# Kernel tuning notes

Hardware: AMD Instinct MI355X
Metric: run time of the kernel (lower is better)

Reference implementation:

```python
import jax, jax.numpy as jnp
import numpy as np

B, N, M, D = 32, 1024, 256, 512
NEG_INF = -1e9  # keras Softmax mask additive constant


def _length_mask(key, batch, length):
    # realistic padding masks: first L positions valid, L >= length//4
    lens = jax.random.randint(key, (batch,), length // 4, length + 1)
    return jnp.arange(length)[None, :] < lens[:, None]


def setup_inputs() -> dict:
    key = jax.random.key(0)
    k1, k2, k3, k4, k5 = jax.random.split(key, 5)
    context = jax.random.normal(k1, (B, N, D), dtype=jnp.float32)
    query = jax.random.normal(k2, (B, M, D), dtype=jnp.float32)
    c_mask = _length_mask(k3, B, N)
    q_mask = _length_mask(k4, B, M)
    # Dense(units=1, use_bias=False) kernel over concat([q, c, q*c]) -> (3D, 1)
    w = jax.random.normal(k5, (3 * D, 1), dtype=jnp.float32) * (1.0 / np.sqrt(3 * D))
    return {"context": context, "query": query, "c_mask": c_mask, "q_mask": q_mask, "w": w}


def reference(context, query, c_mask, q_mask, w):
    d = context.shape[-1]
    # stack order in original: [q_matrix, c_matrix, q*c]
    w_q = w[:d, 0]
    w_c = w[d:2 * d, 0]
    w_m = w[2 * d:, 0]
    # trilinear similarity S[b,n,m] = q_j.w_q + c_i.w_c + (c_i*q_j).w_m, decomposed
    S = (context @ w_c)[:, :, None] \
        + (query @ w_q)[:, None, :] \
        + jnp.einsum('bnd,bmd->bnm', context * w_m, query)
    # context-direction softmax over query axis (axis=2), masked by q_mask
    A = jax.nn.softmax(jnp.where(q_mask[:, None, :], S, NEG_INF), axis=2)
    # query-direction softmax over context axis (axis=1), masked by c_mask
    Bm = jax.nn.softmax(jnp.where(c_mask[:, :, None], S, NEG_INF), axis=1)
    # context-to-query attention: A @ query -> (b, n, d)
    c2q = jnp.einsum('bnm,bmd->bnd', A, query)
    # query-to-context: (A @ B^T) @ context -> (b, n, d)
    q2c = jnp.einsum('bnk,bjk,bjd->bnd', A, Bm, context)
    out = jnp.concatenate([context, c2q, context * c2q, context * q2c], axis=-1)
    return out
```

## Files before the change

kernel.cpp:

```cpp
#include <hip/hip_runtime.h>
#include <hip/hip_bf16.h>

#define B_ 32
#define N_ 1024
#define M_ 256
#define D_ 512

typedef __attribute__((ext_vector_type(8))) short short8;
typedef __attribute__((ext_vector_type(4))) float f32x4;

#define OFF_S     ((size_t)0)
#define OFF_CTXW  ((size_t)8388608)
#define OFF_ANM   ((size_t)8388608)
#define OFF_BMT   ((size_t)12582912)
#define OFF_QB    ((size_t)16777216)
#define OFF_QT    ((size_t)18874368)
#define OFF_CT    ((size_t)20971520)
#define OFF_CDOT  ((size_t)29360128)
#define OFF_QDOT  ((size_t)29392896)
#define OFF_PMAX  ((size_t)29483008)
#define OFF_PSUM  ((size_t)29614080)
#define OFF_RPMAX ((size_t)29745152)
#define OFF_RPSUM ((size_t)29876224)

__global__ __launch_bounds__(256) void prep_all(
    const float* __restrict__ ctx, const float* __restrict__ qry,
    const float* __restrict__ w,
    __hip_bfloat16* __restrict__ ctxw, __hip_bfloat16* __restrict__ cT,
    float* __restrict__ cdot,
    __hip_bfloat16* __restrict__ qb, __hip_bfloat16* __restrict__ qT,
    float* __restrict__ qdot)
{
    __shared__ float t[64][65];
    const int b = blockIdx.z, d0 = blockIdx.x * 64;
    const int tid = threadIdx.x;
    const float* src;
    __hip_bfloat16* rowdst;
    __hip_bfloat16* trdst;
    float* dotdst;
    int ldt;
    float4 wmv, wdv;
    const int lr16 = tid & 15, rband = tid >> 4;
    const int c = lr16 * 4;
    if (blockIdx.y < N_ / 64) {
        int r0 = blockIdx.y * 64;
        src    = ctx + ((size_t)b * N_ + r0) * D_ + d0;
        rowdst = ctxw + ((size_t)b * N_ + r0) * D_ + d0;
        trdst  = cT + ((size_t)b * D_ + d0) * N_ + r0;
        dotdst = cdot + b * N_ + r0;
        wmv = *(const float4*)(w + 2 * D_ + d0 + c);
        wdv = *(const float4*)(w + D_ + d0 + c);
        ldt = N_;
    } else {
        int r0 = (blockIdx.y - N_ / 64) * 64;
        src    = qry + ((size_t)b * M_ + r0) * D_ + d0;
        rowdst = qb + ((size_t)b * M_ + r0) * D_ + d0;
        trdst  = qT + ((size_t)b * D_ + d0) * M_ + r0;
        dotdst = qdot + b * M_ + r0;
        wmv = (float4){1.f, 1.f, 1.f, 1.f};
        wdv = *(const float4*)(w + d0 + c);
        ldt = M_;
    }
#pragma unroll
    for (int i = 0; i < 4; ++i) {
        int r = i * 16 + rband;
        float4 x = *(const float4*)(src + (size_t)r * D_ + c);
        t[r][c] = x.x; t[r][c + 1] = x.y; t[r][c + 2] = x.z; t[r][c + 3] = x.w;
        __hip_bfloat16 o[4] __attribute__((aligned(8)));
        o[0] = __float2bfloat16(x.x * wmv.x);
        o[1] = __float2bfloat16(x.y * wmv.y);
        o[2] = __float2bfloat16(x.z * wmv.z);
        o[3] = __float2bfloat16(x.w * wmv.w);
        *(ushort4*)(rowdst + (size_t)r * D_ + c) = *(ushort4*)o;
        float p = x.x * wdv.x + x.y * wdv.y + x.z * wdv.z + x.w * wdv.w;
#pragma unroll
        for (int off = 1; off < 16; off <<= 1) p += __shfl_xor(p, off, 64);
        if (lr16 == 0) atomicAdd(dotdst + r, p);
    }
    __syncthreads();
    const int dr = tid >> 2, sseg = tid & 3;
    __hip_bfloat16 o[16] __attribute__((aligned(16)));
#pragma unroll
    for (int j = 0; j < 16; ++j)
        o[j] = __float2bfloat16(t[sseg * 16 + j][dr]);
    __hip_bfloat16* dp = trdst + (size_t)dr * ldt + sseg * 16;
    ((short8*)dp)[0] = ((short8*)o)[0];
    ((short8*)dp)[1] = ((short8*)o)[1];
}


__device__ __forceinline__ void gl2lds16(const __hip_bfloat16* g, __hip_bfloat16* l) {
    __builtin_amdgcn_global_load_lds(
        (const __attribute__((address_space(1))) unsigned int*)g,
        (__attribute__((address_space(3))) unsigned int*)l, 16, 0, 0);
}

template<int KTOT>
__device__ __forceinline__ void mfma128(
    const __hip_bfloat16* __restrict__ Abase, int lda,
    const __hip_bfloat16* __restrict__ Bbase, int ldb,
    __hip_bfloat16* As, __hip_bfloat16* Bs, f32x4 acc[4][4])
{
    const int tid = threadIdx.x;
    const int w = tid >> 6, lane = tid & 63;
    const int quad = lane >> 4, lr = lane & 15;
    const int wr = w >> 1, wc = w & 1;
    const int srow = w * 32 + (lane >> 2);
    const int scol = (lane & 3) * 8;
    const __hip_bfloat16* ga0 = Abase + (size_t)srow * lda + scol;
    const __hip_bfloat16* ga1 = ga0 + (size_t)16 * lda;
    const __hip_bfloat16* gb0 = Bbase + (size_t)srow * ldb + scol;
    const __hip_bfloat16* gb1 = gb0 + (size_t)16 * ldb;
    __hip_bfloat16* la0 = As + w * 1024;
    __hip_bfloat16* la1 = As + w * 1024 + 512;
    __hip_bfloat16* lb0 = Bs + w * 1024;
    __hip_bfloat16* lb1 = Bs + w * 1024 + 512;
    const int aoff = (wr * 64 + lr) * 32 + quad * 8;
    const int boff = (wc * 64 + lr) * 32 + quad * 8;

    for (int k0 = 0; k0 < KTOT; k0 += 32) {
        gl2lds16(ga0, la0); gl2lds16(ga1, la1);
        gl2lds16(gb0, lb0); gl2lds16(gb1, lb1);
        ga0 += 32; ga1 += 32; gb0 += 32; gb1 += 32;
        asm volatile("s_waitcnt vmcnt(0)" ::: "memory");
        __syncthreads();
        short8 a[4], bb[4];
        const short8* ap = (const short8*)(As + aoff);
        const short8* bp = (const short8*)(Bs + boff);
#pragma unroll
        for (int fi = 0; fi < 4; ++fi) a[fi] = ap[fi * 64];
#pragma unroll
        for (int fj = 0; fj < 4; ++fj) bb[fj] = bp[fj * 64];
#pragma unroll
        for (int fi = 0; fi < 4; ++fi)
#pragma unroll
            for (int fj = 0; fj < 4; ++fj)
                acc[fi][fj] = __builtin_amdgcn_mfma_f32_16x16x32_bf16(
                    a[fi], bb[fj], acc[fi][fj], 0, 0, 0);
        __syncthreads();
    }
}

template<int KTOT>
__device__ __forceinline__ void mfma128x2(
    const __hip_bfloat16* __restrict__ Abase, int lda,
    const __hip_bfloat16* __restrict__ B1base,
    const __hip_bfloat16* __restrict__ B2base, int ldb,
    __hip_bfloat16* As, __hip_bfloat16* B1s, __hip_bfloat16* B2s,
    f32x4 acc1[4][4], f32x4 acc2[4][4])
{
    const int tid = threadIdx.x;
    const int w = tid >> 6, lane = tid & 63;
    const int quad = lane >> 4, lr = lane & 15;
    const int wr = w >> 1, wc = w & 1;
    const int srow = w * 32 + (lane >> 2);
    const int scol = (lane & 3) * 8;
    const __hip_bfloat16* ga0 = Abase + (size_t)srow * lda + scol;
    const __hip_bfloat16* ga1 = ga0 + (size_t)16 * lda;
    const __hip_bfloat16* gb10 = B1base + (size_t)srow * ldb + scol;
    const __hip_bfloat16* gb11 = gb10 + (size_t)16 * ldb;
    const __hip_bfloat16* gb20 = B2base + (size_t)srow * ldb + scol;
    const __hip_bfloat16* gb21 = gb20 + (size_t)16 * ldb;
    __hip_bfloat16* la0 = As + w * 1024;
    __hip_bfloat16* la1 = la0 + 512;
    __hip_bfloat16* lb10 = B1s + w * 1024;
    __hip_bfloat16* lb11 = lb10 + 512;
    __hip_bfloat16* lb20 = B2s + w * 1024;
    __hip_bfloat16* lb21 = lb20 + 512;
    const int aoff = (wr * 64 + lr) * 32 + quad * 8;
    const int boff = (wc * 64 + lr) * 32 + quad * 8;

    for (int k0 = 0; k0 < KTOT; k0 += 32) {
        gl2lds16(ga0, la0); gl2lds16(ga1, la1);
        gl2lds16(gb10, lb10); gl2lds16(gb11, lb11);
        gl2lds16(gb20, lb20); gl2lds16(gb21, lb21);
        ga0 += 32; ga1 += 32; gb10 += 32; gb11 += 32; gb20 += 32; gb21 += 32;
        asm volatile("s_waitcnt vmcnt(0)" ::: "memory");
        __syncthreads();
        short8 a[4], b1[4], b2[4];
        const short8* ap = (const short8*)(As + aoff);
        const short8* bp1 = (const short8*)(B1s + boff);
        const short8* bp2 = (const short8*)(B2s + boff);
#pragma unroll
        for (int fi = 0; fi < 4; ++fi) a[fi] = ap[fi * 64];
#pragma unroll
        for (int fj = 0; fj < 4; ++fj) { b1[fj] = bp1[fj * 64]; b2[fj] = bp2[fj * 64]; }
#pragma unroll
        for (int fi = 0; fi < 4; ++fi)
#pragma unroll
            for (int fj = 0; fj < 4; ++fj) {
                acc1[fi][fj] = __builtin_amdgcn_mfma_f32_16x16x32_bf16(
                    a[fi], b1[fj], acc1[fi][fj], 0, 0, 0);
                acc2[fi][fj] = __builtin_amdgcn_mfma_f32_16x16x32_bf16(
                    a[fi], b2[fj], acc2[fi][fj], 0, 0, 0);
            }
        __syncthreads();
    }
}

#define ACC_INIT(acc) \
    _Pragma("unroll") for (int i_ = 0; i_ < 4; ++i_) \
    _Pragma("unroll") for (int j_ = 0; j_ < 4; ++j_) acc[i_][j_] = (f32x4){0.f, 0.f, 0.f, 0.f};

#define EPI_IDX const int tid = threadIdx.x, lane = tid & 63, quad = lane >> 4, lr = lane & 15; \
    const int wr = tid >> 7, wc = (tid >> 6) & 1;

__global__ __launch_bounds__(256) void s_gemm_stats(
    const __hip_bfloat16* __restrict__ ctxw, const __hip_bfloat16* __restrict__ qryb,
    const float* __restrict__ cdot, const float* __restrict__ qdot,
    const int* __restrict__ q_mask, const int* __restrict__ c_mask,
    float* __restrict__ S,
    float* __restrict__ rpmax, float* __restrict__ rpsum,
    float* __restrict__ pmax, float* __restrict__ psum)
{
    __shared__ __align__(16) __hip_bfloat16 As[4096], Bs[4096];
    const int b = blockIdx.z, n0 = blockIdx.y * 128, m0 = blockIdx.x * 128;
    f32x4 acc[4][4];
    ACC_INIT(acc)
    mfma128<512>(ctxw + ((size_t)b * N_ + n0) * D_, D_,
                 qryb + ((size_t)b * M_ + m0) * D_, D_, As, Bs, acc);
    EPI_IDX
    float cd[4][4]; int cmv[4][4];
#pragma unroll
    for (int fi = 0; fi < 4; ++fi)
#pragma unroll
        for (int r = 0; r < 4; ++r) {
            int n = n0 + wr * 64 + fi * 16 + quad * 4 + r;
            cd[fi][r] = cdot[b * N_ + n];
            cmv[fi][r] = c_mask[b * N_ + n];
        }
    float qd[4]; int qmv[4];
#pragma unroll
    for (int fj = 0; fj < 4; ++fj) {
        int m = m0 + wc * 64 + fj * 16 + lr;
        qd[fj] = qdot[b * M_ + m];
        qmv[fj] = q_mask[b * M_ + m];
    }
#pragma unroll
    for (int fi = 0; fi < 4; ++fi)
#pragma unroll
        for (int r = 0; r < 4; ++r) {
            int n = n0 + wr * 64 + fi * 16 + quad * 4 + r;
            size_t rowoff = ((size_t)b * N_ + n) * M_;
#pragma unroll
            for (int fj = 0; fj < 4; ++fj) {
                int m = m0 + wc * 64 + fj * 16 + lr;
                S[rowoff + m] = acc[fi][fj][r] + cd[fi][r] + qd[fj];
            }
        }
    const int part = blockIdx.x * 2 + wc;
#pragma unroll
    for (int fi = 0; fi < 4; ++fi)
#pragma unroll
        for (int r = 0; r < 4; ++r) {
            float xs[4], mx = -1e30f;
#pragma unroll
            for (int fj = 0; fj < 4; ++fj) {
                xs[fj] = qmv[fj] ? (acc[fi][fj][r] + cd[fi][r] + qd[fj]) : -1e9f;
                mx = fmaxf(mx, xs[fj]);
            }
#pragma unroll
            for (int off = 1; off < 16; off <<= 1)
                mx = fmaxf(mx, __shfl_xor(mx, off, 64));
            float se = 0.f;
#pragma unroll
            for (int fj = 0; fj < 4; ++fj) se += __expf(xs[fj] - mx);
#pragma unroll
            for (int off = 1; off < 16; off <<= 1)
                se += __shfl_xor(se, off, 64);
            if (lr == 0) {
                int n = n0 + wr * 64 + fi * 16 + quad * 4 + r;
                rpmax[((size_t)b * N_ + n) * 4 + part] = mx;
                rpsum[((size_t)b * N_ + n) * 4 + part] = se;
            }
        }
    const int ch = blockIdx.y * 2 + wr;
#pragma unroll
    for (int fj = 0; fj < 4; ++fj) {
        float mx = -1e30f;
#pragma unroll
        for (int fi = 0; fi < 4; ++fi)
#pragma unroll
            for (int r = 0; r < 4; ++r) {
                float x = cmv[fi][r] ? (acc[fi][fj][r] + cd[fi][r] + qd[fj]) : -1e9f;
                mx = fmaxf(mx, x);
            }
        mx = fmaxf(mx, __shfl_xor(mx, 16, 64));
        mx = fmaxf(mx, __shfl_xor(mx, 32, 64));
        float se = 0.f;
#pragma unroll
        for (int fi = 0; fi < 4; ++fi)
#pragma unroll
            for (int r = 0; r < 4; ++r) {
                float x = cmv[fi][r] ? (acc[fi][fj][r] + cd[fi][r] + qd[fj]) : -1e9f;
                se += __expf(x - mx);
            }
        se += __shfl_xor(se, 16, 64);
        se += __shfl_xor(se, 32, 64);
        if (lane < 16) {
            int m = m0 + wc * 64 + fj * 16 + lr;
            pmax[((size_t)b * 16 + ch) * M_ + m] = mx;
            psum[((size_t)b * 16 + ch) * M_ + m] = se;
        }
    }
}

__global__ __launch_bounds__(256) void q2cpart_mfma(
    const __hip_bfloat16* __restrict__ ctxT, const __hip_bfloat16* __restrict__ BmT,
    __hip_bfloat16* __restrict__ Q2CT)
{
    __shared__ __align__(16) __hip_bfloat16 As[4096], Bs[4096];
    const int b = blockIdx.z, d0 = blockIdx.y * 128, m0 = blockIdx.x * 128;
    f32x4 acc[4][4];
    ACC_INIT(acc)
    mfma128<1024>(ctxT + ((size_t)b * D_ + d0) * N_, N_,
                  BmT + ((size_t)b * M_ + m0) * N_, N_, As, Bs, acc);
    EPI_IDX
#pragma unroll
    for (int fi = 0; fi < 4; ++fi) {
#pragma unroll
        for (int r = 0; r < 4; ++r) {
            int d = d0 + wr * 64 + fi * 16 + quad * 4 + r;
#pragma unroll
            for (int fj = 0; fj < 4; ++fj) {
                int m = m0 + wc * 64 + fj * 16 + lr;
                Q2CT[((size_t)b * D_ + d) * M_ + m] = __float2bfloat16(acc[fi][fj][r]);
            }
        }
    }
}

__global__ __launch_bounds__(256) void out_fused_mfma(
    const __hip_bfloat16* __restrict__ Anm, const __hip_bfloat16* __restrict__ qryT,
    const __hip_bfloat16* __restrict__ Q2CT, const float* __restrict__ ctx,
    float* __restrict__ out)
{
    __shared__ __align__(16) __hip_bfloat16 As[4096], B1s[4096], B2s[4096];
    const int b = blockIdx.z, n0 = blockIdx.y * 128, d0 = blockIdx.x * 128;
    f32x4 acc1[4][4], acc2[4][4];
    ACC_INIT(acc1)
    ACC_INIT(acc2)
    mfma128x2<256>(Anm + ((size_t)b * N_ + n0) * M_, M_,
                   qryT + ((size_t)b * D_ + d0) * M_,
                   Q2CT + ((size_t)b * D_ + d0) * M_, M_,
                   As, B1s, B2s, acc1, acc2);
    EPI_IDX
#pragma unroll
    for (int fi = 0; fi < 4; ++fi) {
#pragma unroll
        for (int r = 0; r < 4; ++r) {
            int n = n0 + wr * 64 + fi * 16 + quad * 4 + r;
            size_t ibase = ((size_t)b * N_ + n) * D_;
            size_t obase = ((size_t)b * N_ + n) * (4 * D_);
#pragma unroll
            for (int fj = 0; fj < 4; ++fj) {
                int d = d0 + wc * 64 + fj * 16 + lr;
                float c = ctx[ibase + d];
                float v1 = acc1[fi][fj][r];
                float v2 = acc2[fi][fj][r];
                out[obase + d] = c;
                out[obase + D_ + d] = v1;
                out[obase + 2 * D_ + d] = c * v1;
                out[obase + 3 * D_ + d] = c * v2;
            }
        }
    }
}

__global__ __launch_bounds__(256) void normalize_kernel(
    const float* __restrict__ S, __hip_bfloat16* __restrict__ Anm,
    __hip_bfloat16* __restrict__ BmT,
    const int* __restrict__ q_mask, const int* __restrict__ c_mask,
    const float* __restrict__ pmax, const float* __restrict__ psum,
    const float* __restrict__ rpmax, const float* __restrict__ rpsum)
{
    __shared__ float t[64][65];
    __shared__ float cmx_s[64], cinv_s[64], rmx_s[64], rinv_s[64];
    const int b = blockIdx.z, n0 = blockIdx.y * 64, m0 = blockIdx.x * 64;
    const int tid = threadIdx.x;
    if (tid < 64) {
        int m = m0 + tid;
        float mx = -1e30f;
#pragma unroll
        for (int ch = 0; ch < 16; ++ch)
            mx = fmaxf(mx, pmax[((size_t)b * 16 + ch) * M_ + m]);
        float sm = 0.f;
#pragma unroll
        for (int ch = 0; ch < 16; ++ch)
            sm += psum[((size_t)b * 16 + ch) * M_ + m] *
                  __expf(pmax[((size_t)b * 16 + ch) * M_ + m] - mx);
        cmx_s[tid] = mx; cinv_s[tid] = 1.0f / sm;
    } else if (tid < 128) {
        int rl = tid - 64;
        size_t row = (size_t)b * N_ + n0 + rl;
        float mx = -1e30f;
#pragma unroll
        for (int p = 0; p < 4; ++p)
            mx = fmaxf(mx, rpmax[row * 4 + p]);
        float sm = 0.f;
#pragma unroll
        for (int p = 0; p < 4; ++p)
            sm += rpsum[row * 4 + p] * __expf(rpmax[row * 4 + p] - mx);
        rmx_s[rl] = mx; rinv_s[rl] = 1.0f / sm;
    }
    __syncthreads();
    const int lr16 = tid & 15, rband = tid >> 4;
    const int c = lr16 * 4;
    int4 qm4 = *(const int4*)(q_mask + b * M_ + m0 + c);
    float cmx0 = cmx_s[c], cmx1 = cmx_s[c + 1], cmx2 = cmx_s[c + 2], cmx3 = cmx_s[c + 3];
    float ci0 = cinv_s[c], ci1 = cinv_s[c + 1], ci2 = cinv_s[c + 2], ci3 = cinv_s[c + 3];
#pragma unroll
    for (int i = 0; i < 4; ++i) {
        int r = i * 16 + rband;
        int n = n0 + r;
        int cm = c_mask[b * N_ + n];
        float rmx = rmx_s[r], rinv = rinv_s[r];
        size_t idx = ((size_t)b * N_ + n) * M_ + m0 + c;
        float4 s4 = *(const float4*)(S + idx);
        __hip_bfloat16 av[4] __attribute__((aligned(8)));
        av[0] = __float2bfloat16(qm4.x ? __expf(s4.x - rmx) * rinv : 0.f);
        av[1] = __float2bfloat16(qm4.y ? __expf(s4.y - rmx) * rinv : 0.f);
        av[2] = __float2bfloat16(qm4.z ? __expf(s4.z - rmx) * rinv : 0.f);
        av[3] = __float2bfloat16(qm4.w ? __expf(s4.w - rmx) * rinv : 0.f);
        *(ushort4*)(Anm + idx) = *(ushort4*)av;
        t[r][c]     = cm ? __expf(s4.x - cmx0) * ci0 : 0.f;
        t[r][c + 1] = cm ? __expf(s4.y - cmx1) * ci1 : 0.f;
        t[r][c + 2] = cm ? __expf(s4.z - cmx2) * ci2 : 0.f;
        t[r][c + 3] = cm ? __expf(s4.w - cmx3) * ci3 : 0.f;
    }
    __syncthreads();
    const int mr = tid >> 2, sseg = tid & 3;
    __hip_bfloat16 o[16] __attribute__((aligned(16)));
#pragma unroll
    for (int j = 0; j < 16; ++j)
        o[j] = __float2bfloat16(t[sseg * 16 + j][mr]);
    __hip_bfloat16* dp = BmT + ((size_t)b * M_ + m0 + mr) * N_ + n0 + sseg * 16;
    ((short8*)dp)[0] = ((short8*)o)[0];
    ((short8*)dp)[1] = ((short8*)o)[1];
}

extern "C" void kernel_launch(void* const* d_in, const int* in_sizes, int n_in,
                              void* d_out, int out_size, void* d_ws, size_t ws_size,
                              hipStream_t stream) {
    const float* ctx   = (const float*)d_in[0];
    const float* qry   = (const float*)d_in[1];
    const int*   cmask = (const int*)d_in[2];
    const int*   qmask = (const int*)d_in[3];
    const float* w     = (const float*)d_in[4];
    float* out = (float*)d_out;
    float* ws  = (float*)d_ws;

    float* S = ws + OFF_S;
    __hip_bfloat16* ctxw = (__hip_bfloat16*)(ws + OFF_CTXW);
    __hip_bfloat16* Anm  = (__hip_bfloat16*)(ws + OFF_ANM);
    __hip_bfloat16* BmT  = (__hip_bfloat16*)(ws + OFF_BMT);
    __hip_bfloat16* qb   = (__hip_bfloat16*)(ws + OFF_QB);
    __hip_bfloat16* Q2CT = (__hip_bfloat16*)(ws + OFF_QB);
    __hip_bfloat16* qT   = (__hip_bfloat16*)(ws + OFF_QT);
    __hip_bfloat16* cT   = (__hip_bfloat16*)(ws + OFF_CT);
    float* cdot = ws + OFF_CDOT;
    float* qdot = ws + OFF_QDOT;
    float* pmax = ws + OFF_PMAX;
    float* psum = ws + OFF_PSUM;
    float* rpmax = ws + OFF_RPMAX;
    float* rpsum = ws + OFF_RPSUM;

    hipMemsetAsync(cdot, 0, (size_t)(B_ * N_ + B_ * M_) * sizeof(float), stream);

    dim3 gp(D_ / 64, (N_ + M_) / 64, B_);
    prep_all<<<gp, 256, 0, stream>>>(ctx, qry, w, ctxw, cT, cdot, qb, qT, qdot);

    dim3 gS(M_ / 128, N_ / 128, B_);
    s_gemm_stats<<<gS, 256, 0, stream>>>(ctxw, qb, cdot, qdot, qmask, cmask,
                                         S, rpmax, rpsum, pmax, psum);

    dim3 gN(M_ / 64, N_ / 64, B_);
    normalize_kernel<<<gN, 256, 0, stream>>>(S, Anm, BmT, qmask, cmask,
                                             pmax, psum, rpmax, rpsum);

    dim3 gP(M_ / 128, D_ / 128, B_);
    q2cpart_mfma<<<gP, 256, 0, stream>>>(cT, BmT, Q2CT);

    dim3 gO(D_ / 128, N_ / 128, B_);
    out_fused_mfma<<<gO, 256, 0, stream>>>(Anm, qT, Q2CT, ctx, out);
}
```

Baseline: 482.0 us.

## Fuse full-row softmax into S GEMM, store bf16 numerators instead of fp32 S

The score GEMM now gives each block a full 128x256 row tile with 512 threads, so it can finish the row-softmax max and sum in-block and write unnormalized exp numerators as bf16 rather than an fp32 S matrix. Row normalization (1/sum) is deferred to the output kernel's epilogue, and the column softmax is rebuilt from the stored numerators by rescaling with exp(rowmax - colmax). This removes the fp32 S round trip and halves the intermediate traffic. The costs are a larger block with fewer blocks in the grid, and some precision loss, because the column softmax is now derived from bf16 numerators that can underflow where the row max dominates.

After: 473.0 us. Within noise of the previous version (-1.9%).

```diff
diff --git a/kernel.cpp b/kernel.cpp
--- a/kernel.cpp
+++ b/kernel.cpp
@@ -9,9 +9,8 @@
 typedef __attribute__((ext_vector_type(8))) short short8;
 typedef __attribute__((ext_vector_type(4))) float f32x4;
 
-#define OFF_S     ((size_t)0)
+#define OFF_ANUM  ((size_t)0)
 #define OFF_CTXW  ((size_t)8388608)
-#define OFF_ANM   ((size_t)8388608)
 #define OFF_BMT   ((size_t)12582912)
 #define OFF_QB    ((size_t)16777216)
 #define OFF_QT    ((size_t)18874368)
@@ -20,8 +19,8 @@
 #define OFF_QDOT  ((size_t)29392896)
 #define OFF_PMAX  ((size_t)29483008)
 #define OFF_PSUM  ((size_t)29614080)
-#define OFF_RPMAX ((size_t)29745152)
-#define OFF_RPSUM ((size_t)29876224)
+#define OFF_RMAX  ((size_t)29745152)
+#define OFF_RINV  ((size_t)29876224)
 
 __global__ __launch_bounds__(256) void prep_all(
     const float* __restrict__ ctx, const float* __restrict__ qry,
@@ -202,24 +201,56 @@
     _Pragma("unroll") for (int i_ = 0; i_ < 4; ++i_) \
     _Pragma("unroll") for (int j_ = 0; j_ < 4; ++j_) acc[i_][j_] = (f32x4){0.f, 0.f, 0.f, 0.f};
 
-#define EPI_IDX const int tid = threadIdx.x, lane = tid & 63, quad = lane >> 4, lr = lane & 15; \
-    const int wr = tid >> 7, wc = (tid >> 6) & 1;
-
-__global__ __launch_bounds__(256) void s_gemm_stats(
+__global__ __launch_bounds__(512) void s_gemm_full(
     const __hip_bfloat16* __restrict__ ctxw, const __hip_bfloat16* __restrict__ qryb,
     const float* __restrict__ cdot, const float* __restrict__ qdot,
     const int* __restrict__ q_mask, const int* __restrict__ c_mask,
-    float* __restrict__ S,
-    float* __restrict__ rpmax, float* __restrict__ rpsum,
+    __hip_bfloat16* __restrict__ Anum,
+    float* __restrict__ rmax_g, float* __restrict__ rinv_g,
     float* __restrict__ pmax, float* __restrict__ psum)
 {
-    __shared__ __align__(16) __hip_bfloat16 As[4096], Bs[4096];
-    const int b = blockIdx.z, n0 = blockIdx.y * 128, m0 = blockIdx.x * 128;
+    __shared__ __align__(16) __hip_bfloat16 As[4096];
+    __shared__ __align__(16) __hip_bfloat16 Bs[8192];
+    __shared__ float rpm[128][4], rps[128][4];
+    __shared__ float rmx_s[128];
+    const int b = blockIdx.y, n0 = blockIdx.x * 128;
+    const int tid = threadIdx.x;
+    const int w = tid >> 6, lane = tid & 63;
+    const int quad = lane >> 4, lr = lane & 15;
+    const int wr = w >> 2, wc = w & 3;
+    const int srow = tid >> 2, scol = (tid & 3) * 8;
+    const __hip_bfloat16* gA  = ctxw + ((size_t)b * N_ + n0 + srow) * D_ + scol;
+    const __hip_bfloat16* gB0 = qryb + ((size_t)b * M_ + srow) * D_ + scol;
+    const __hip_bfloat16* gB1 = qryb + ((size_t)b * M_ + 128 + srow) * D_ + scol;
+    __hip_bfloat16* la  = As + w * 512;
+    __hip_bfloat16* lb0 = Bs + w * 512;
+    __hip_bfloat16* lb1 = Bs + 4096 + w * 512;
+    const int aoff = (wr * 64 + lr) * 32 + quad * 8;
+    const int boff = (wc * 64 + lr) * 32 + quad * 8;
+
     f32x4 acc[4][4];
     ACC_INIT(acc)
-    mfma128<512>(ctxw + ((size_t)b * N_ + n0) * D_, D_,
-                 qryb + ((size_t)b * M_ + m0) * D_, D_, As, Bs, acc);
-    EPI_IDX
+    for (int k0 = 0; k0 < D_; k0 += 32) {
+        gl2lds16(gA, la); gl2lds16(gB0, lb0); gl2lds16(gB1, lb1);
+        gA += 32; gB0 += 32; gB1 += 32;
+        asm volatile("s_waitcnt vmcnt(0)" ::: "memory");
+        __syncthreads();
+        short8 a[4], bb[4];
+        const short8* ap = (const short8*)(As + aoff);
+        const short8* bp = (const short8*)(Bs + boff);
+#pragma unroll
+        for (int fi = 0; fi < 4; ++fi) a[fi] = ap[fi * 64];
+#pragma unroll
+        for (int fj = 0; fj < 4; ++fj) bb[fj] = bp[fj * 64];
+#pragma unroll
+        for (int fi = 0; fi < 4; ++fi)
+#pragma unroll
+            for (int fj = 0; fj < 4; ++fj)
+                acc[fi][fj] = __builtin_amdgcn_mfma_f32_16x16x32_bf16(
+                    a[fi], bb[fj], acc[fi][fj], 0, 0, 0);
+        __syncthreads();
+    }
+
     float cd[4][4]; int cmv[4][4];
 #pragma unroll
     for (int fi = 0; fi < 4; ++fi)
@@ -232,23 +263,10 @@
     float qd[4]; int qmv[4];
 #pragma unroll
     for (int fj = 0; fj < 4; ++fj) {
-        int m = m0 + wc * 64 + fj * 16 + lr;
+        int m = wc * 64 + fj * 16 + lr;
         qd[fj] = qdot[b * M_ + m];
         qmv[fj] = q_mask[b * M_ + m];
     }
-#pragma unroll
-    for (int fi = 0; fi < 4; ++fi)
-#pragma unroll
-        for (int r = 0; r < 4; ++r) {
-            int n = n0 + wr * 64 + fi * 16 + quad * 4 + r;
-            size_t rowoff = ((size_t)b * N_ + n) * M_;
-#pragma unroll
-            for (int fj = 0; fj < 4; ++fj) {
-                int m = m0 + wc * 64 + fj * 16 + lr;
-                S[rowoff + m] = acc[fi][fj][r] + cd[fi][r] + qd[fj];
-            }
-        }
-    const int part = blockIdx.x * 2 + wc;
 #pragma unroll
     for (int fi = 0; fi < 4; ++fi)
 #pragma unroll
@@ -269,12 +287,38 @@
             for (int off = 1; off < 16; off <<= 1)
                 se += __shfl_xor(se, off, 64);
             if (lr == 0) {
-                int n = n0 + wr * 64 + fi * 16 + quad * 4 + r;
-                rpmax[((size_t)b * N_ + n) * 4 + part] = mx;
-                rpsum[((size_t)b * N_ + n) * 4 + part] = se;
-            }
-        }
-    const int ch = blockIdx.y * 2 + wr;
+                int nl = wr * 64 + fi * 16 + quad * 4 + r;
+                rpm[nl][wc] = mx; rps[nl][wc] = se;
+            }
+        }
+    __syncthreads();
+    if (tid < 128) {
+        float m0v = rpm[tid][0], m1 = rpm[tid][1], m2 = rpm[tid][2], m3 = rpm[tid][3];
+        float mx = fmaxf(fmaxf(m0v, m1), fmaxf(m2, m3));
+        float sm = rps[tid][0] * __expf(m0v - mx) + rps[tid][1] * __expf(m1 - mx)
+                 + rps[tid][2] * __expf(m2 - mx) + rps[tid][3] * __expf(m3 - mx);
+        float inv = 1.0f / sm;
+        rmx_s[tid] = mx;
+        rmax_g[b * N_ + n0 + tid] = mx;
+        rinv_g[b * N_ + n0 + tid] = inv;
+    }
+    __syncthreads();
+#pragma unroll
+    for (int fi = 0; fi < 4; ++fi)
+#pragma unroll
+        for (int r = 0; r < 4; ++r) {
+            int nl = wr * 64 + fi * 16 + quad * 4 + r;
+            float rmx = rmx_s[nl];
+            size_t rowoff = ((size_t)b * N_ + n0 + nl) * M_;
+#pragma unroll
+            for (int fj = 0; fj < 4; ++fj) {
+                int m = wc * 64 + fj * 16 + lr;
+                float sv = acc[fi][fj][r] + cd[fi][r] + qd[fj];
+                float a = qmv[fj] ? __expf(sv - rmx) : 0.f;
+                Anum[rowoff + m] = __float2bfloat16(a);
+            }
+        }
+    const int ch = blockIdx.x * 2 + wr;
 #pragma unroll
     for (int fj = 0; fj < 4; ++fj) {
         float mx = -1e30f;
@@ -298,12 +342,69 @@
         se += __shfl_xor(se, 16, 64);
         se += __shfl_xor(se, 32, 64);
         if (lane < 16) {
-            int m = m0 + wc * 64 + fj * 16 + lr;
+            int m = wc * 64 + fj * 16 + lr;
             pmax[((size_t)b * 16 + ch) * M_ + m] = mx;
             psum[((size_t)b * 16 + ch) * M_ + m] = se;
         }
     }
 }
+
+__global__ __launch_bounds__(256) void normalize_bm(
+    const __hip_bfloat16* __restrict__ Anum, __hip_bfloat16* __restrict__ BmT,
+    const int* __restrict__ c_mask,
+    const float* __restrict__ pmax, const float* __restrict__ psum,
+    const float* __restrict__ rmax_g)
+{
+    __shared__ float t[64][65];
+    __shared__ float cmx_s[64], cinv_s[64], rmx_s[64];
+    const int b = blockIdx.z, n0 = blockIdx.y * 64, m0 = blockIdx.x * 64;
+    const int tid = threadIdx.x;
+    if (tid < 64) {
+        int m = m0 + tid;
+        float mx = -1e30f;
+#pragma unroll
+        for (int ch = 0; ch < 16; ++ch)
+            mx = fmaxf(mx, pmax[((size_t)b * 16 + ch) * M_ + m]);
+        float sm = 0.f;
+#pragma unroll
+        for (int ch = 0; ch < 16; ++ch)
+            sm += psum[((size_t)b * 16 + ch) * M_ + m] *
+                  __expf(pmax[((size_t)b * 16 + ch) * M_ + m] - mx);
+        cmx_s[tid] = mx; cinv_s[tid] = 1.0f / sm;
+    } else if (tid < 128) {
+        int rl = tid - 64;
+        rmx_s[rl] = rmax_g[(size_t)b * N_ + n0 + rl];
+    }
+    __syncthreads();
+    const int lr8 = tid & 7, rband = tid >> 3;
+    const int c = lr8 * 8;
+#pragma unroll
+    for (int i = 0; i < 2; ++i) {
+        int r = i * 32 + rband;
+        int n = n0 + r;
+        int cm = c_mask[b * N_ + n];
+        float rmx = rmx_s[r];
+        short8 a8 = *(const short8*)(Anum + ((size_t)b * N_ + n) * M_ + m0 + c);
+#pragma unroll
+        for (int j = 0; j < 8; ++j) {
+            int ml = c + j;
+            float anv = __bfloat162float(*(const __hip_bfloat16*)&((short*)&a8)[j]);
+            t[r][ml] = cm ? anv * __expf(rmx - cmx_s[ml]) * cinv_s[ml] : 0.f;
+        }
+    }
+    __syncthreads();
+    const int mr = tid >> 2, sseg = tid & 3;
+    __hip_bfloat16 o[16] __attribute__((aligned(16)));
+#pragma unroll
+    for (int j = 0; j < 16; ++j)
+        o[j] = __float2bfloat16(t[sseg * 16 + j][mr]);
+    __hip_bfloat16* dp = BmT + ((size_t)b * M_ + m0 + mr) * N_ + n0 + sseg * 16;
+    ((short8*)dp)[0] = ((short8*)o)[0];
+    ((short8*)dp)[1] = ((short8*)o)[1];
+}
+
+#define EPI_IDX const int tid = threadIdx.x, lane = tid & 63, quad = lane >> 4, lr = lane & 15; \
+    const int wr = tid >> 7, wc = (tid >> 6) & 1;
 
 __global__ __launch_bounds__(256) void q2cpart_mfma(
     const __hip_bfloat16* __restrict__ ctxT, const __hip_bfloat16* __restrict__ BmT,
@@ -331,16 +432,16 @@
 }
 
 __global__ __launch_bounds__(256) void out_fused_mfma(
-    const __hip_bfloat16* __restrict__ Anm, const __hip_bfloat16* __restrict__ qryT,
+    const __hip_bfloat16* __restrict__ Anum, const __hip_bfloat16* __restrict__ qryT,
     const __hip_bfloat16* __restrict__ Q2CT, const float* __restrict__ ctx,
-    float* __restrict__ out)
+    const float* __restrict__ rinv_g, float* __restrict__ out)
 {
     __shared__ __align__(16) __hip_bfloat16 As[4096], B1s[4096], B2s[4096];
     const int b = blockIdx.z, n0 = blockIdx.y * 128, d0 = blockIdx.x * 128;
     f32x4 acc1[4][4], acc2[4][4];
     ACC_INIT(acc1)
     ACC_INIT(acc2)
-    mfma128x2<256>(Anm + ((size_t)b * N_ + n0) * M_, M_,
+    mfma128x2<256>(Anum + ((size_t)b * N_ + n0) * M_, M_,
                    qryT + ((size_t)b * D_ + d0) * M_,
                    Q2CT + ((size_t)b * D_ + d0) * M_, M_,
                    As, B1s, B2s, acc1, acc2);
@@ -350,14 +451,15 @@
 #pragma unroll
         for (int r = 0; r < 4; ++r) {
             int n = n0 + wr * 64 + fi * 16 + quad * 4 + r;
+            float rinv = rinv_g[(size_t)b * N_ + n];
             size_t ibase = ((size_t)b * N_ + n) * D_;
             size_t obase = ((size_t)b * N_ + n) * (4 * D_);
 #pragma unroll
             for (int fj = 0; fj < 4; ++fj) {
                 int d = d0 + wc * 64 + fj * 16 + lr;
                 float c = ctx[ibase + d];
-                float v1 = acc1[fi][fj][r];
-                float v2 = acc2[fi][fj][r];
+                float v1 = acc1[fi][fj][r] * rinv;
+                float v2 = acc2[fi][fj][r] * rinv;
                 out[obase + d] = c;
                 out[obase + D_ + d] = v1;
                 out[obase + 2 * D_ + d] = c * v1;
@@ -365,78 +467,6 @@
             }
         }
     }
-}
-
-__global__ __launch_bounds__(256) void normalize_kernel(
-    const float* __restrict__ S, __hip_bfloat16* __restrict__ Anm,
-    __hip_bfloat16* __restrict__ BmT,
-    const int* __restrict__ q_mask, const int* __restrict__ c_mask,
-    const float* __restrict__ pmax, const float* __restrict__ psum,
-    const float* __restrict__ rpmax, const float* __restrict__ rpsum)
-{
-    __shared__ float t[64][65];
-    __shared__ float cmx_s[64], cinv_s[64], rmx_s[64], rinv_s[64];
-    const int b = blockIdx.z, n0 = blockIdx.y * 64, m0 = blockIdx.x * 64;
-    const int tid = threadIdx.x;
-    if (tid < 64) {
-        int m = m0 + tid;
-        float mx = -1e30f;
-#pragma unroll
-        for (int ch = 0; ch < 16; ++ch)
-            mx = fmaxf(mx, pmax[((size_t)b * 16 + ch) * M_ + m]);
-        float sm = 0.f;
-#pragma unroll
-        for (int ch = 0; ch < 16; ++ch)
-            sm += psum[((size_t)b * 16 + ch) * M_ + m] *
-                  __expf(pmax[((size_t)b * 16 + ch) * M_ + m] - mx);
-        cmx_s[tid] = mx; cinv_s[tid] = 1.0f / sm;
-    } else if (tid < 128) {
-        int rl = tid - 64;
-        size_t row = (size_t)b * N_ + n0 + rl;
-        float mx = -1e30f;
-#pragma unroll
-        for (int p = 0; p < 4; ++p)
-            mx = fmaxf(mx, rpmax[row * 4 + p]);
-        float sm = 0.f;
-#pragma unroll
-        for (int p = 0; p < 4; ++p)
-            sm += rpsum[row * 4 + p] * __expf(rpmax[row * 4 + p] - mx);
-        rmx_s[rl] = mx; rinv_s[rl] = 1.0f / sm;
-    }
-    __syncthreads();
-    const int lr16 = tid & 15, rband = tid >> 4;
-    const int c = lr16 * 4;
-    int4 qm4 = *(const int4*)(q_mask + b * M_ + m0 + c);
-    float cmx0 = cmx_s[c], cmx1 = cmx_s[c + 1], cmx2 = cmx_s[c + 2], cmx3 = cmx_s[c + 3];
-    float ci0 = cinv_s[c], ci1 = cinv_s[c + 1], ci2 = cinv_s[c + 2], ci3 = cinv_s[c + 3];
-#pragma unroll
-    for (int i = 0; i < 4; ++i) {
-        int r = i * 16 + rband;
-        int n = n0 + r;
-        int cm = c_mask[b * N_ + n];
-        float rmx = rmx_s[r], rinv = rinv_s[r];
-        size_t idx = ((size_t)b * N_ + n) * M_ + m0 + c;
-        float4 s4 = *(const float4*)(S + idx);
-        __hip_bfloat16 av[4] __attribute__((aligned(8)));
-        av[0] = __float2bfloat16(qm4.x ? __expf(s4.x - rmx) * rinv : 0.f);
-        av[1] = __float2bfloat16(qm4.y ? __expf(s4.y - rmx) * rinv : 0.f);
-        av[2] = __float2bfloat16(qm4.z ? __expf(s4.z - rmx) * rinv : 0.f);
-        av[3] = __float2bfloat16(qm4.w ? __expf(s4.w - rmx) * rinv : 0.f);
-        *(ushort4*)(Anm + idx) = *(ushort4*)av;
-        t[r][c]     = cm ? __expf(s4.x - cmx0) * ci0 : 0.f;
-        t[r][c + 1] = cm ? __expf(s4.y - cmx1) * ci1 : 0.f;
-        t[r][c + 2] = cm ? __expf(s4.z - cmx2) * ci2 : 0.f;
-        t[r][c + 3] = cm ? __expf(s4.w - cmx3) * ci3 : 0.f;
-    }
-    __syncthreads();
-    const int mr = tid >> 2, sseg = tid & 3;
-    __hip_bfloat16 o[16] __attribute__((aligned(16)));
-#pragma unroll
-    for (int j = 0; j < 16; ++j)
-        o[j] = __float2bfloat16(t[sseg * 16 + j][mr]);
-    __hip_bfloat16* dp = BmT + ((size_t)b * M_ + m0 + mr) * N_ + n0 + sseg * 16;
-    ((short8*)dp)[0] = ((short8*)o)[0];
-    ((short8*)dp)[1] = ((short8*)o)[1];
 }
 
 extern "C" void kernel_launch(void* const* d_in, const int* in_sizes, int n_in,
@@ -450,9 +480,8 @@
     float* out = (float*)d_out;
     float* ws  = (float*)d_ws;
 
-    float* S = ws + OFF_S;
+    __hip_bfloat16* Anum = (__hip_bfloat16*)(ws + OFF_ANUM);
     __hip_bfloat16* ctxw = (__hip_bfloat16*)(ws + OFF_CTXW);
-    __hip_bfloat16* Anm  = (__hip_bfloat16*)(ws + OFF_ANM);
     __hip_bfloat16* BmT  = (__hip_bfloat16*)(ws + OFF_BMT);
     __hip_bfloat16* qb   = (__hip_bfloat16*)(ws + OFF_QB);
     __hip_bfloat16* Q2CT = (__hip_bfloat16*)(ws + OFF_QB);
@@ -462,25 +491,24 @@
     float* qdot = ws + OFF_QDOT;
     float* pmax = ws + OFF_PMAX;
     float* psum = ws + OFF_PSUM;
-    float* rpmax = ws + OFF_RPMAX;
-    float* rpsum = ws + OFF_RPSUM;
+    float* rmax = ws + OFF_RMAX;
+    float* rinv = ws + OFF_RINV;
 
     hipMemsetAsync(cdot, 0, (size_t)(B_ * N_ + B_ * M_) * sizeof(float), stream);
 
     dim3 gp(D_ / 64, (N_ + M_) / 64, B_);
     prep_all<<<gp, 256, 0, stream>>>(ctx, qry, w, ctxw, cT, cdot, qb, qT, qdot);
 
-    dim3 gS(M_ / 128, N_ / 128, B_);
-    s_gemm_stats<<<gS, 256, 0, stream>>>(ctxw, qb, cdot, qdot, qmask, cmask,
-                                         S, rpmax, rpsum, pmax, psum);
+    dim3 gS(N_ / 128, B_);
+    s_gemm_full<<<gS, 512, 0, stream>>>(ctxw, qb, cdot, qdot, qmask, cmask,
+                                        Anum, rmax, rinv, pmax, psum);
 
     dim3 gN(M_ / 64, N_ / 64, B_);
-    normalize_kernel<<<gN, 256, 0, stream>>>(S, Anm, BmT, qmask, cmask,
-                                             pmax, psum, rpmax, rpsum);
+    normalize_bm<<<gN, 256, 0, stream>>>(Anum, BmT, cmask, pmax, psum, rmax);
 
     dim3 gP(M_ / 128, D_ / 128, B_);
     q2cpart_mfma<<<gP, 256, 0, stream>>>(cT, BmT, Q2CT);
 
     dim3 gO(D_ / 128, N_ / 128, B_);
-    out_fused_mfma<<<gO, 256, 0, stream>>>(Anm, qT, Q2CT, ctx, out);
-}
+    out_fused_mfma<<<gO, 256, 0, stream>>>(Anum, qT, Q2CT, ctx, rinv, out);
+}
```
